# Optimization experiments

Hardware: AMD Instinct MI355X
Metric: run time of the kernel (lower is better)

Reference implementation:

```python
import jax, jax.numpy as jnp
import numpy as np
import math

B, T, S, C, E = 8, 2048, 2048, 1024, 1024

def setup_inputs() -> dict:
    key = jax.random.key(0)
    ks = jax.random.split(key, 6)
    x = jax.random.normal(ks[0], (B, T, C), dtype=jnp.float32)
    tgt = jax.random.normal(ks[1], (B, T, E), dtype=jnp.float32)
    enc_a = jax.random.normal(ks[2], (B, E, S), dtype=jnp.float32)
    enc_b = jax.random.normal(ks[3], (B, S, E), dtype=jnp.float32)
    mask = jax.random.randint(ks[4], (B, S), 0, 2).astype(bool)
    w_in = jax.random.normal(ks[5], (E, C), dtype=jnp.float32) * math.sqrt(1.0 / C)
    b_in = jnp.zeros((E,), dtype=jnp.float32)
    w_out = jax.random.normal(jax.random.fold_in(key, 7), (C, E), dtype=jnp.float32) * math.sqrt(1.0 / E)
    b_out = jnp.zeros((C,), dtype=jnp.float32)
    return {"x": x, "target_embedding": tgt, "encoder_a": enc_a, "encoder_b": enc_b,
            "encoder_padding_mask": mask, "w_in": w_in, "b_in": b_in,
            "w_out": w_out, "b_out": b_out}

def reference(x, target_embedding, encoder_a, encoder_b, encoder_padding_mask,
              w_in, b_in, w_out, b_out):
    residual = x
    h = (jnp.einsum('btc,ec->bte', x, w_in) + b_in + target_embedding) * math.sqrt(0.5)
    # attention scores: [B, T, S]
    scores = jnp.einsum('bte,bes->bts', h, encoder_a)
    scores = jnp.where(encoder_padding_mask[:, None, :], -jnp.inf, scores)
    attn = jax.nn.softmax(scores, axis=-1)
    out = jnp.einsum('bts,bse->bte', attn, encoder_b)
    s = encoder_b.shape[1]
    out = out * (s * math.sqrt(1.0 / s))
    out = (jnp.einsum('bte,ce->btc', out, w_out) + b_out + residual) * math.sqrt(0.5)
    return (out, attn)
```

## Files before the change

kernel.cpp:

```cpp
#include <hip/hip_runtime.h>
#include <hip/hip_bf16.h>
#include <math.h>

#define NB 8
#define TT 2048
#define SS 2048
#define CC 1024
#define EE 1024
#define NMAX 1280

typedef __attribute__((ext_vector_type(8))) short short8;
typedef __attribute__((ext_vector_type(4))) float f32x4;

__device__ __forceinline__ unsigned short f2bf(float f) {
  unsigned u = __builtin_bit_cast(unsigned, f);
  u += 0x7fffu + ((u >> 16) & 1u);
  return (unsigned short)(u >> 16);
}
__device__ __forceinline__ float bf2f(unsigned short h) {
  unsigned u = ((unsigned)h) << 16;
  return __builtin_bit_cast(float, u);
}
__device__ __forceinline__ void gload16(const void* g, void* l) {
  __builtin_amdgcn_global_load_lds((const __attribute__((address_space(1))) void*)g,
                                   (__attribute__((address_space(3))) void*)l, 16, 0, 0);
}
__device__ __forceinline__ unsigned ldsoff(const void* p) {
  return (unsigned)(size_t)(const __attribute__((address_space(3))) char*)p;
}
__device__ __forceinline__ short8 ds128(unsigned off) {
  short8 r;
  asm volatile("ds_read_b128 %0, %1" : "=v"(r) : "v"(off));
  return r;
}
__device__ __forceinline__ int swzi(int x) { return x ^ (((x >> 7) & 7) << 4); }

#define WAITV(N) asm volatile("s_waitcnt vmcnt(" #N ")" ::: "memory")
#define WAITL(N) asm volatile("s_waitcnt lgkmcnt(" #N ")" ::: "memory")
#define BAR() __builtin_amdgcn_s_barrier()
#define SCH0() __builtin_amdgcn_sched_barrier(0)
#define PRIO1() __builtin_amdgcn_s_setprio(1)
#define PRIO0() __builtin_amdgcn_s_setprio(0)
#define MF(a_, b_, c_) __builtin_amdgcn_mfma_f32_16x16x32_bf16(a_, b_, c_, 0, 0, 0)

__device__ __forceinline__ int xcd_logical() {
  int gx = gridDim.x, gy = gridDim.y, gz = gridDim.z;
  int pid = blockIdx.x + gx * (blockIdx.y + gy * blockIdx.z);
  int q = (gx * gy * gz) >> 3;
  return (pid & 7) * q + (pid >> 3);
}

__global__ __launch_bounds__(256) void k_scan(const int* __restrict__ mask,
    int* __restrict__ idx, int* __restrict__ pfx, int* __restrict__ cnt,
    int* __restrict__ kpad) {
  __shared__ int cs[256];
  int b = blockIdx.x, t = threadIdx.x;
  const int* mrow = mask + (size_t)b * SS;
  int4 a = ((const int4*)mrow)[t * 2];
  int4 c2 = ((const int4*)mrow)[t * 2 + 1];
  int mm[8] = {a.x, a.y, a.z, a.w, c2.x, c2.y, c2.z, c2.w};
  int c = 0;
#pragma unroll
  for (int j = 0; j < 8; ++j) c += (mm[j] == 0);
  cs[t] = c;
  __syncthreads();
  if (t == 0) {
    int run = 0;
    for (int i = 0; i < 256; ++i) { int tmp = cs[i]; cs[i] = run; run += tmp; }
    cnt[b] = run;
    int kp = (run + 127) & ~127;
    if (kp > NMAX) kp = NMAX;
    kpad[b] = kp;
  }
  __syncthreads();
  int base = cs[t];
#pragma unroll
  for (int j = 0; j < 8; ++j) {
    int s = t * 8 + j;
    pfx[(size_t)b * SS + s] = base;
    if (mm[j] == 0) { idx[(size_t)b * SS + base] = s; base++; }
  }
}

__global__ __launch_bounds__(256) void k_split(const float* __restrict__ in,
    unsigned short* __restrict__ hi, unsigned short* __restrict__ lo, long n4) {
  long i = (long)blockIdx.x * blockDim.x + threadIdx.x;
  long stride = (long)gridDim.x * blockDim.x;
  for (; i < n4; i += stride) {
    float4 v = ((const float4*)in)[i];
    float f[4] = {v.x, v.y, v.z, v.w};
    unsigned short hh[4], ll[4];
#pragma unroll
    for (int j = 0; j < 4; ++j) {
      hh[j] = f2bf(f[j]);
      ll[j] = f2bf(f[j] - bf2f(hh[j]));
    }
    ushort4 h; h.x = hh[0]; h.y = hh[1]; h.z = hh[2]; h.w = hh[3];
    ushort4 l; l.x = ll[0]; l.y = ll[1]; l.z = ll[2]; l.w = ll[3];
    ((ushort4*)hi)[i] = h;
    ((ushort4*)lo)[i] = l;
  }
}

__global__ __launch_bounds__(256) void k_conv(const float* __restrict__ in,
    unsigned short* __restrict__ out, long n4) {
  long i = (long)blockIdx.x * blockDim.x + threadIdx.x;
  long stride = (long)gridDim.x * blockDim.x;
  for (; i < n4; i += stride) {
    float4 v = ((const float4*)in)[i];
    ushort4 h; h.x = f2bf(v.x); h.y = f2bf(v.y); h.z = f2bf(v.z); h.w = f2bf(v.w);
    ((ushort4*)out)[i] = h;
  }
}

__global__ __launch_bounds__(256) void k_ta(const float* __restrict__ enca,
    const int* __restrict__ idx, const int* __restrict__ cnt,
    unsigned short* __restrict__ hi, unsigned short* __restrict__ lo) {
  __shared__ float tile[64][65];
  int b = blockIdx.z, sc0 = blockIdx.x * 64, e0 = blockIdx.y * 64;
  int cb = cnt[b];
  const float* src = enca + (size_t)b * EE * SS;
  int t = threadIdx.x, tr = t >> 4, tc = (t & 15) * 4;
  int idxv[4];
#pragma unroll
  for (int j = 0; j < 4; ++j) {
    int sc = sc0 + tc + j;
    idxv[j] = (sc < cb) ? idx[(size_t)b * SS + sc] : -1;
  }
#pragma unroll
  for (int i = 0; i < 4; ++i) {
    int e = tr + i * 16;
#pragma unroll
    for (int j = 0; j < 4; ++j)
      tile[e][tc + j] = (idxv[j] >= 0) ? src[(size_t)(e0 + e) * SS + idxv[j]] : 0.f;
  }
  __syncthreads();
  size_t ob = (size_t)b * NMAX * EE;
#pragma unroll
  for (int i = 0; i < 4; ++i) {
    int c = tr + i * 16;
    unsigned short hh[4], ll[4];
#pragma unroll
    for (int j = 0; j < 4; ++j) {
      float f = tile[tc + j][c];
      hh[j] = f2bf(f);
      ll[j] = f2bf(f - bf2f(hh[j]));
    }
    ushort4 h; h.x = hh[0]; h.y = hh[1]; h.z = hh[2]; h.w = hh[3];
    ushort4 l; l.x = ll[0]; l.y = ll[1]; l.z = ll[2]; l.w = ll[3];
    *(ushort4*)(hi + ob + (size_t)(sc0 + c) * EE + e0 + tc) = h;
    *(ushort4*)(lo + ob + (size_t)(sc0 + c) * EE + e0 + tc) = l;
  }
}

__global__ __launch_bounds__(256) void k_tb(const float* __restrict__ encb,
    const int* __restrict__ idx, const int* __restrict__ cnt,
    unsigned short* __restrict__ out) {
  __shared__ float tile[64][65];
  int b = blockIdx.z, sc0 = blockIdx.x * 64, e0 = blockIdx.y * 64;
  int cb = cnt[b];
  const float* src = encb + (size_t)b * SS * EE;
  int t = threadIdx.x, tr = t >> 4, tc = (t & 15) * 4;
#pragma unroll
  for (int i = 0; i < 4; ++i) {
    int r = tr + i * 16;
    int sc = sc0 + r;
    int sidx = (sc < cb) ? idx[(size_t)b * SS + sc] : -1;
    float4 v;
    if (sidx >= 0) v = *(const float4*)(src + (size_t)sidx * EE + e0 + tc);
    else { v.x = v.y = v.z = v.w = 0.f; }
    tile[r][tc] = v.x; tile[r][tc + 1] = v.y; tile[r][tc + 2] = v.z; tile[r][tc + 3] = v.w;
  }
  __syncthreads();
  size_t ob = (size_t)b * EE * NMAX;
#pragma unroll
  for (int i = 0; i < 4; ++i) {
    int c = tr + i * 16;
    unsigned short hh[4];
#pragma unroll
    for (int j = 0; j < 4; ++j) hh[j] = f2bf(tile[tc + j][c]);
    ushort4 h; h.x = hh[0]; h.y = hh[1]; h.z = hh[2]; h.w = hh[3];
    *(ushort4*)(out + ob + (size_t)(e0 + c) * NMAX + sc0 + tc) = h;
  }
}

template <int EPI>
__global__ __launch_bounds__(512, 2) void k_gemm8(
    const unsigned short* __restrict__ A, const unsigned short* __restrict__ B,
    int N, int KROW, const int* __restrict__ kdyn, long sA, long sB, long sC,
    const float* __restrict__ bias, const float* __restrict__ addend,
    float* __restrict__ outF, unsigned short* __restrict__ outH, float scale) {
  extern __shared__ char lds[];
  const int tid = threadIdx.x, wave = tid >> 6, lane = tid & 63;
  int L = xcd_logical();
  const int n0 = (L % gridDim.x) * 256;
  int tmpL = L / gridDim.x;
  const int m0 = (tmpL % gridDim.y) * 256;
  const int b = tmpL / gridDim.y;
  const int KD = kdyn ? kdyn[b] : KROW;
  const int wm = wave >> 2, wn = wave & 3;
  const unsigned short* gA = A + (size_t)b * sA + (size_t)m0 * KROW;
  const unsigned short* gB = B + (size_t)b * sB + (size_t)n0 * KROW;
  const unsigned ldsB = ldsoff(lds);

  int srow[2], sk8[2];
#pragma unroll
  for (int s = 0; s < 2; ++s) {
    int l = swzi((s * 512 + tid) * 16);
    srow[s] = l >> 6;
    sk8[s] = (l >> 4) & 3;
  }
  const int aR = wm * 128 + (lane & 15);
  const int bR = wn * 64 + (lane & 15);
  const int kB = (lane >> 4) * 16;
  const int nkt = KD >> 6;

  f32x4 acc[8][4] = {};

  auto STG = [&](int t, int tensor, int ks) {
    const unsigned short* g = tensor ? gB : gA;
    char* dst = lds + (t & 1) * 65536 + tensor * 32768 + ks * 16384 + wave * 1024;
    size_t gk = (size_t)t * 64 + ks * 32;
#pragma unroll
    for (int s = 0; s < 2; ++s)
      gload16(g + ((size_t)srow[s] * KROW + gk + sk8[s] * 8), dst + s * 8192);
  };
  auto RA = [&](int t, int ks, int mf) {
    int lin = (aR + mf * 16) * 64 + kB;
    return ds128(ldsB + (t & 1) * 65536 + ks * 16384 + swzi(lin));
  };
  auto RB = [&](int t, int ks, int nf) {
    int lin = (bR + nf * 16) * 64 + kB;
    return ds128(ldsB + (t & 1) * 65536 + 32768 + ks * 16384 + swzi(lin));
  };

  STG(0, 1, 0); STG(0, 0, 0); STG(0, 0, 1); STG(0, 1, 1);
  if (nkt > 1) { STG(1, 1, 0); STG(1, 0, 0); }

  for (int u = 0; u < nkt; ++u) {
    if (u + 1 < nkt) { WAITV(8); } else { WAITV(0); }
    BAR();
    short8 bf[4], af[4];
#pragma unroll
    for (int nf = 0; nf < 4; ++nf) bf[nf] = RB(u, 0, nf);
#pragma unroll
    for (int mf = 0; mf < 4; ++mf) af[mf] = RA(u, 0, mf);
    if (u + 1 < nkt) { STG(u + 1, 0, 1); STG(u + 1, 1, 1); }
    BAR(); WAITL(0); SCH0(); PRIO1();
#pragma unroll
    for (int mf = 0; mf < 4; ++mf)
#pragma unroll
      for (int nf = 0; nf < 4; ++nf) acc[mf][nf] = MF(af[mf], bf[nf], acc[mf][nf]);
    PRIO0(); SCH0(); BAR();
#pragma unroll
    for (int mf = 0; mf < 4; ++mf) af[mf] = RA(u, 0, mf + 4);
    if (u + 2 < nkt) STG(u + 2, 1, 0);
    BAR(); WAITL(0); SCH0(); PRIO1();
#pragma unroll
    for (int mf = 0; mf < 4; ++mf)
#pragma unroll
      for (int nf = 0; nf < 4; ++nf) acc[mf + 4][nf] = MF(af[mf], bf[nf], acc[mf + 4][nf]);
    PRIO0(); SCH0();
    if (u + 2 < nkt) { WAITV(10); } else if (u + 1 < nkt) { WAITV(8); } else { WAITV(0); }
    BAR();
#pragma unroll
    for (int nf = 0; nf < 4; ++nf) bf[nf] = RB(u, 1, nf);
#pragma unroll
    for (int mf = 0; mf < 4; ++mf) af[mf] = RA(u, 1, mf);
    if (u + 2 < nkt) STG(u + 2, 0, 0);
    BAR(); WAITL(0); SCH0(); PRIO1();
#pragma unroll
    for (int mf = 0; mf < 4; ++mf)
#pragma unroll
      for (int nf = 0; nf < 4; ++nf) acc[mf][nf] = MF(af[mf], bf[nf], acc[mf][nf]);
    PRIO0(); SCH0(); BAR();
#pragma unroll
    for (int mf = 0; mf < 4; ++mf) af[mf] = RA(u, 1, mf + 4);
    BAR(); WAITL(0); SCH0(); PRIO1();
#pragma unroll
    for (int mf = 0; mf < 4; ++mf)
#pragma unroll
      for (int nf = 0; nf < 4; ++nf) acc[mf + 4][nf] = MF(af[mf], bf[nf], acc[mf + 4][nf]);
    PRIO0(); SCH0(); BAR();
  }

  const size_t cb = (size_t)b * sC;
  const int mB = m0 + wm * 128 + ((lane >> 4) << 2);
  const int nB = n0 + wn * 64 + (lane & 15);
#pragma unroll
  for (int mf = 0; mf < 8; ++mf)
#pragma unroll
    for (int j = 0; j < 4; ++j) {
      int m = mB + mf * 16 + j;
#pragma unroll
      for (int nf = 0; nf < 4; ++nf) {
        int n = nB + nf * 16;
        float v = acc[mf][nf][j];
        size_t o = (size_t)m * N + n;
        if (EPI == 2) outH[cb + o] = f2bf(v * scale);
        else outF[o] = (v + bias[n] + addend[o]) * scale;
      }
    }
}

template <int EPI>
__global__ __launch_bounds__(512, 2) void k_split8(
    const unsigned short* __restrict__ Ah, const unsigned short* __restrict__ Al,
    const unsigned short* __restrict__ Bh, const unsigned short* __restrict__ Bl,
    int N, int K, long sA, long sB, long sC,
    const float* __restrict__ bias, const float* __restrict__ addend,
    float* __restrict__ outF, unsigned short* __restrict__ outHi,
    unsigned short* __restrict__ outLo, float scale, const int* __restrict__ npad) {
  extern __shared__ char lds[];
  const int tid = threadIdx.x, wave = tid >> 6, lane = tid & 63;
  int L = xcd_logical();
  const int n0 = (L % gridDim.x) * 256;
  int tmpL = L / gridDim.x;
  const int m0 = (tmpL % gridDim.y) * 256;
  const int b = tmpL / gridDim.y;
  if (npad && n0 >= npad[b]) return;
  const int wm = wave >> 2, wn = wave & 3;
  const unsigned short* gb[4];
  gb[0] = Ah + (size_t)b * sA + (size_t)m0 * K;
  gb[1] = Al + (size_t)b * sA + (size_t)m0 * K;
  gb[2] = Bh + (size_t)b * sB + (size_t)n0 * K;
  gb[3] = Bl + (size_t)b * sB + (size_t)n0 * K;
  const unsigned ldsB = ldsoff(lds);

  int soff[2];
#pragma unroll
  for (int s = 0; s < 2; ++s) {
    int l = swzi((s * 512 + tid) * 16);
    soff[s] = (l >> 6) * K + ((l >> 4) & 3) * 8;
  }
  const int aR = wm * 128 + (lane & 15);
  const int bR = wn * 64 + (lane & 15);
  const int kB = (lane >> 4) * 16;
  const int nkt = K >> 5;

  unsigned vA = ldsB + (unsigned)swzi(aR * 64 + kB);
  unsigned vB = ldsB + (unsigned)swzi(bR * 64 + kB);

  f32x4 acc[8][4] = {};

  auto STG2 = [&](int t, unsigned bufbase, int region) {
    char* dst = lds + bufbase + region * 16384 + tid * 16;
    const unsigned short* g = gb[region] + (size_t)t * 32;
#pragma unroll
    for (int s = 0; s < 2; ++s)
      gload16(g + soff[s], dst + s * 8192);
  };

#define PH_TOP() BAR()
#define PH_MID() BAR(); WAITL(0); SCH0(); PRIO1()
#define PH_END() PRIO0(); SCH0()

#define TILE(u, WV1, WV3, WV5, STAGE) do {                                     \
  short8 ahi[8], bhi[4], blo[4], alo[4];                                       \
                                                         \
  WV1; PH_TOP();                                                               \
  _Pragma("unroll") for (int q = 0; q < 4; ++q) bhi[q] = ds128(vB + 32768 + q * 1024); \
  _Pragma("unroll") for (int q = 0; q < 4; ++q) ahi[q] = ds128(vA + q * 1024); \
  if (STAGE) STG2((u) + 1, nbuf, 0);                                           \
  PH_MID();                                                                    \
  _Pragma("unroll") for (int mi = 0; mi < 4; ++mi)                             \
  _Pragma("unroll") for (int ni = 0; ni < 4; ++ni)                             \
    acc[mi][ni] = MF(ahi[mi], bhi[ni], acc[mi][ni]);                           \
  PH_END();                                                                    \
                                                         \
  PH_TOP();                                                                    \
  _Pragma("unroll") for (int q = 0; q < 4; ++q) ahi[4 + q] = ds128(vA + (4 + q) * 1024); \
  if (STAGE) STG2((u) + 1, nbuf, 2);                                           \
  PH_MID();                                                                    \
  _Pragma("unroll") for (int mi = 0; mi < 4; ++mi)                             \
  _Pragma("unroll") for (int ni = 0; ni < 4; ++ni)                             \
    acc[4 + mi][ni] = MF(ahi[4 + mi], bhi[ni], acc[4 + mi][ni]);               \
  PH_END();                                                                    \
                                                         \
  WV3; PH_TOP();                                                               \
  _Pragma("unroll") for (int q = 0; q < 4; ++q) blo[q] = ds128(vB + 49152 + q * 1024); \
  if (STAGE) STG2((u) + 1, nbuf, 3);                                           \
  PH_MID();                                                                    \
  _Pragma("unroll") for (int mi = 0; mi < 4; ++mi)                             \
  _Pragma("unroll") for (int ni = 0; ni < 4; ++ni)                             \
    acc[mi][ni] = MF(ahi[mi], blo[ni], acc[mi][ni]);                           \
  PH_END();                                                                    \
                                                         \
  PH_TOP();                                                                    \
  if (STAGE) STG2((u) + 1, nbuf, 1);                                           \
  PH_MID();                                                                    \
  _Pragma("unroll") for (int mi = 0; mi < 4; ++mi)                             \
  _Pragma("unroll") for (int ni = 0; ni < 4; ++ni)                             \
    acc[4 + mi][ni] = MF(ahi[4 + mi], blo[ni], acc[4 + mi][ni]);               \
  PH_END();                                                                    \
                                                         \
  WV5; PH_TOP();                                                               \
  _Pragma("unroll") for (int q = 0; q < 4; ++q) alo[q] = ds128(vA + 16384 + q * 1024); \
  PH_MID();                                                                    \
  _Pragma("unroll") for (int mi = 0; mi < 4; ++mi)                             \
  _Pragma("unroll") for (int ni = 0; ni < 4; ++ni)                             \
    acc[mi][ni] = MF(alo[mi], bhi[ni], acc[mi][ni]);                           \
  PH_END();                                                                    \
                                                         \
  PH_TOP();                                                                    \
  _Pragma("unroll") for (int q = 0; q < 4; ++q) alo[q] = ds128(vA + 16384 + (4 + q) * 1024); \
  PH_MID();                                                                    \
  _Pragma("unroll") for (int mi = 0; mi < 4; ++mi)                             \
  _Pragma("unroll") for (int ni = 0; ni < 4; ++ni)                             \
    acc[4 + mi][ni] = MF(alo[mi], bhi[ni], acc[4 + mi][ni]);                   \
  PH_END();                                                                    \
  vA ^= 65536u; vB ^= 65536u;                                                  \
} while (0)

  STG2(0, 0, 0); STG2(0, 0, 2); STG2(0, 0, 3); STG2(0, 0, 1);

  unsigned nbuf = 65536u;
  for (int u = 0; u < nkt - 1; ++u) {
    TILE(u, WAITV(4), WAITV(6), WAITV(8), 1);
    nbuf ^= 65536u;
  }
  TILE(nkt - 1, WAITV(4), WAITV(2), WAITV(0), 0);
#undef TILE
#undef PH_TOP
#undef PH_MID
#undef PH_END

  const size_t cb = (size_t)b * sC;
  const int mB = m0 + wm * 128 + ((lane >> 4) << 2);
  const int nB = n0 + wn * 64 + (lane & 15);
#pragma unroll
  for (int mf = 0; mf < 8; ++mf)
#pragma unroll
    for (int j = 0; j < 4; ++j) {
      int m = mB + mf * 16 + j;
#pragma unroll
      for (int nf = 0; nf < 4; ++nf) {
        int n = nB + nf * 16;
        float v = acc[mf][nf][j];
        size_t o = (size_t)m * N + n;
        if (EPI == 0) {
          v = (v + bias[n] + addend[o]) * scale;
          unsigned short hb = f2bf(v);
          outHi[o] = hb;
          outLo[o] = f2bf(v - bf2f(hb));
        } else {
          outF[cb + o] = v;
        }
      }
    }
}

__global__ __launch_bounds__(256) void k_softmax(const float* __restrict__ scores_c,
    float* __restrict__ attn, unsigned short* __restrict__ attn_bc,
    const int* __restrict__ mask, const int* __restrict__ pfx,
    const int* __restrict__ cnt, const int* __restrict__ kpad) {
  __shared__ float sl[NMAX];
  __shared__ float red[8];
  long r = blockIdx.x;
  int b = (int)(r >> 11);
  int t = threadIdx.x;
  int cb = cnt[b], kp = kpad[b];
  const float* srow = scores_c + r * (long)NMAX;
  for (int i = t; i < cb; i += 256) sl[i] = srow[i];
  __syncthreads();
  int base = t * 8;
  const int* mrow = mask + (size_t)b * SS;
  int4 m0i = *(const int4*)(mrow + base);
  int4 m1i = *(const int4*)(mrow + base + 4);
  int mm[8] = {m0i.x, m0i.y, m0i.z, m0i.w, m1i.x, m1i.y, m1i.z, m1i.w};
  const int* prow = pfx + (size_t)b * SS;
  int4 p0i = *(const int4*)(prow + base);
  int4 p1i = *(const int4*)(prow + base + 4);
  int pp[8] = {p0i.x, p0i.y, p0i.z, p0i.w, p1i.x, p1i.y, p1i.z, p1i.w};
  float v[8];
#pragma unroll
  for (int j = 0; j < 8; ++j) v[j] = mm[j] ? -INFINITY : sl[pp[j]];
  float mx = v[0];
#pragma unroll
  for (int j = 1; j < 8; ++j) mx = fmaxf(mx, v[j]);
#pragma unroll
  for (int off = 32; off; off >>= 1) mx = fmaxf(mx, __shfl_xor(mx, off));
  int wv = t >> 6, ln = t & 63;
  if (ln == 0) red[wv] = mx;
  __syncthreads();
  mx = fmaxf(fmaxf(red[0], red[1]), fmaxf(red[2], red[3]));
  float sum = 0.f;
#pragma unroll
  for (int j = 0; j < 8; ++j) { v[j] = __expf(v[j] - mx); sum += v[j]; }
#pragma unroll
  for (int off = 32; off; off >>= 1) sum += __shfl_xor(sum, off);
  if (ln == 0) red[4 + wv] = sum;
  __syncthreads();
  sum = (red[4] + red[5]) + (red[6] + red[7]);
  float inv = 1.0f / sum;
#pragma unroll
  for (int j = 0; j < 8; ++j) v[j] *= inv;
  float* arow = attn + r * (long)SS;
  float4 w0; w0.x = v[0]; w0.y = v[1]; w0.z = v[2]; w0.w = v[3];
  float4 w1; w1.x = v[4]; w1.y = v[5]; w1.z = v[6]; w1.w = v[7];
  *(float4*)(arow + base) = w0;
  *(float4*)(arow + base + 4) = w1;
  __syncthreads();
#pragma unroll
  for (int j = 0; j < 8; ++j) if (!mm[j]) sl[pp[j]] = v[j];
  __syncthreads();
  unsigned short* brow = attn_bc + r * (long)NMAX;
  for (int i = t; i < kp; i += 256) brow[i] = f2bf(i < cb ? sl[i] : 0.f);
}

extern "C" void kernel_launch(void* const* d_in, const int* in_sizes, int n_in,
                              void* d_out, int out_size, void* d_ws, size_t ws_size,
                              hipStream_t stream) {
  (void)in_sizes; (void)n_in; (void)out_size; (void)ws_size;
  const float* x     = (const float*)d_in[0];
  const float* tgt   = (const float*)d_in[1];
  const float* enca  = (const float*)d_in[2];
  const float* encb  = (const float*)d_in[3];
  const int*   mask  = (const int*)d_in[4];
  const float* w_in  = (const float*)d_in[5];
  const float* b_in  = (const float*)d_in[6];
  const float* w_out = (const float*)d_in[7];
  const float* b_out = (const float*)d_in[8];

  float* out  = (float*)d_out;
  float* attn = out + (size_t)NB * TT * CC;

  char* ws = (char*)d_ws;
  float*          scores_c = (float*)(ws + 0);
  unsigned short* x_hi   = (unsigned short*)(ws + 0);
  unsigned short* x_lo   = (unsigned short*)(ws + 33554432L);
  unsigned short* pv     = (unsigned short*)(ws + 0);
  unsigned short* h_hi   = (unsigned short*)(ws + 83886080L);
  unsigned short* h_lo   = (unsigned short*)(ws + 117440512L);
  unsigned short* attn_bc= (unsigned short*)(ws + 83886080L);
  unsigned short* a_tc_hi= (unsigned short*)(ws + 150994944L);
  unsigned short* a_tc_lo= (unsigned short*)(ws + 171966464L);
  unsigned short* b_tc   = (unsigned short*)(ws + 192937984L);
  unsigned short* w_in_hi= (unsigned short*)(ws + 213909504L);
  unsigned short* w_in_lo= (unsigned short*)(ws + 216006656L);
  unsigned short* w_out_b= (unsigned short*)(ws + 218103808L);
  int* idx  = (int*)(ws + 220200960L);
  int* pfx  = (int*)(ws + 220266496L);
  int* cnt  = (int*)(ws + 220332032L);
  int* kpad = (int*)(ws + 220332096L);

  hipFuncSetAttribute(reinterpret_cast<const void*>(&k_gemm8<2>),
                      hipFuncAttributeMaxDynamicSharedMemorySize, 131072);
  hipFuncSetAttribute(reinterpret_cast<const void*>(&k_gemm8<3>),
                      hipFuncAttributeMaxDynamicSharedMemorySize, 131072);
  hipFuncSetAttribute(reinterpret_cast<const void*>(&k_split8<0>),
                      hipFuncAttributeMaxDynamicSharedMemorySize, 131072);
  hipFuncSetAttribute(reinterpret_cast<const void*>(&k_split8<1>),
                      hipFuncAttributeMaxDynamicSharedMemorySize, 131072);

  dim3 blk(256), blk512(512);
  const float S05 = 0.70710678118654752f;

  k_scan<<<NB, blk, 0, stream>>>(mask, idx, pfx, cnt, kpad);
  k_split<<<2048, blk, 0, stream>>>(x, x_hi, x_lo, (long)NB * TT * CC / 4);
  k_split<<<512, blk, 0, stream>>>(w_in, w_in_hi, w_in_lo, (long)EE * CC / 4);
  k_conv<<<512, blk, 0, stream>>>(w_out, w_out_b, (long)CC * EE / 4);
  k_ta<<<dim3(NMAX / 64, EE / 64, NB), blk, 0, stream>>>(enca, idx, cnt, a_tc_hi, a_tc_lo);
  k_tb<<<dim3(NMAX / 64, EE / 64, NB), blk, 0, stream>>>(encb, idx, cnt, b_tc);

  k_split8<0><<<dim3(EE / 256, (NB * TT) / 256, 1), blk512, 131072, stream>>>(
      x_hi, x_lo, w_in_hi, w_in_lo, EE, CC, 0, 0, 0,
      b_in, tgt, nullptr, h_hi, h_lo, S05, nullptr);

  k_split8<1><<<dim3(NMAX / 256, TT / 256, NB), blk512, 131072, stream>>>(
      h_hi, h_lo, a_tc_hi, a_tc_lo, NMAX, EE,
      (long)TT * EE, (long)NMAX * EE, (long)TT * NMAX,
      nullptr, nullptr, scores_c, nullptr, nullptr, 1.0f, kpad);

  k_softmax<<<NB * TT, blk, 0, stream>>>(scores_c, attn, attn_bc, mask, pfx, cnt, kpad);

  k_gemm8<2><<<dim3(EE / 256, TT / 256, NB), blk512, 131072, stream>>>(
      attn_bc, b_tc, EE, NMAX, kpad,
      (long)TT * NMAX, (long)EE * NMAX, (long)TT * EE,
      nullptr, nullptr, nullptr, pv, 45.254833995939045f);

  k_gemm8<3><<<dim3(CC / 256, (NB * TT) / 256, 1), blk512, 131072, stream>>>(
      pv, w_out_b, CC, EE, nullptr, 0, 0, 0,
      b_out, x, out, nullptr, S05);
}
```

Baseline: 511.1 us.

## Shrink split-bf16 GEMM tile to 128x256 with single-buffered three-phase pipeline

Changes the split-precision (hi/lo bf16) GEMM kernel from 256x256 tiles with a double-buffered 128KB LDS pipeline to 128x256 tiles using a 48KB single-buffer scheme. Loads for the next k-step are interleaved into the three MFMA phases. Per-wave accumulators drop from 8x4 to 4x4. The goal is lower register and LDS pressure, higher occupancy and more blocks for better load balance. The cost is less A/B reuse per tile, more global traffic, and possible exposed latency with only one buffer.

```diff
diff --git a/kernel.cpp b/kernel.cpp
--- a/kernel.cpp
+++ b/kernel.cpp
@@ -316,7 +316,7 @@
   int L = xcd_logical();
   const int n0 = (L % gridDim.x) * 256;
   int tmpL = L / gridDim.x;
-  const int m0 = (tmpL % gridDim.y) * 256;
+  const int m0 = (tmpL % gridDim.y) * 128;
   const int b = tmpL / gridDim.y;
   if (npad && n0 >= npad[b]) return;
   const int wm = wave >> 2, wn = wave & 3;
@@ -327,109 +327,77 @@
   gb[3] = Bl + (size_t)b * sB + (size_t)n0 * K;
   const unsigned ldsB = ldsoff(lds);
 
-  int soff[2];
+  int aoff, boff[2];
+  { int l = swzi(tid * 16); aoff = (l >> 6) * K + ((l >> 4) & 3) * 8; }
 #pragma unroll
   for (int s = 0; s < 2; ++s) {
-    int l = swzi((s * 512 + tid) * 16);
-    soff[s] = (l >> 6) * K + ((l >> 4) & 3) * 8;
-  }
-  const int aR = wm * 128 + (lane & 15);
+    int l = swzi(s * 8192 + tid * 16);
+    boff[s] = (l >> 6) * K + ((l >> 4) & 3) * 8;
+  }
+  const int aR = wm * 64 + (lane & 15);
   const int bR = wn * 64 + (lane & 15);
   const int kB = (lane >> 4) * 16;
   const int nkt = K >> 5;
 
-  unsigned vA = ldsB + (unsigned)swzi(aR * 64 + kB);
-  unsigned vB = ldsB + (unsigned)swzi(bR * 64 + kB);
-
-  f32x4 acc[8][4] = {};
-
-  auto STG2 = [&](int t, unsigned bufbase, int region) {
-    char* dst = lds + bufbase + region * 16384 + tid * 16;
-    const unsigned short* g = gb[region] + (size_t)t * 32;
-#pragma unroll
-    for (int s = 0; s < 2; ++s)
-      gload16(g + soff[s], dst + s * 8192);
+  const unsigned vA = ldsB + (unsigned)swzi(aR * 64 + kB);
+  const unsigned vB = ldsB + 16384u + (unsigned)swzi(bR * 64 + kB);
+
+  f32x4 acc[4][4] = {};
+
+  auto STG_A = [&](int t, int r) {
+    gload16(gb[r] + (size_t)t * 32 + aoff, lds + r * 8192 + tid * 16);
   };
-
-#define PH_TOP() BAR()
-#define PH_MID() BAR(); WAITL(0); SCH0(); PRIO1()
-#define PH_END() PRIO0(); SCH0()
-
-#define TILE(u, WV1, WV3, WV5, STAGE) do {                                     \
-  short8 ahi[8], bhi[4], blo[4], alo[4];                                       \
-                                                         \
-  WV1; PH_TOP();                                                               \
-  _Pragma("unroll") for (int q = 0; q < 4; ++q) bhi[q] = ds128(vB + 32768 + q * 1024); \
+  auto STG_B = [&](int t, int r) {
+    char* base = lds + 16384 + (r - 2) * 16384;
+    const unsigned short* g = gb[r] + (size_t)t * 32;
+    gload16(g + boff[0], base + tid * 16);
+    gload16(g + boff[1], base + 8192 + tid * 16);
+  };
+
+#define TILE3(u, WV1, WV2, WV3, STAGE) do {                                    \
+  short8 ahi[4], bhi[4], blo[4], alo[4];                                       \
+                                                               \
+  WV1; BAR();                                                                  \
+  _Pragma("unroll") for (int q = 0; q < 4; ++q) bhi[q] = ds128(vB + q * 1024); \
   _Pragma("unroll") for (int q = 0; q < 4; ++q) ahi[q] = ds128(vA + q * 1024); \
-  if (STAGE) STG2((u) + 1, nbuf, 0);                                           \
-  PH_MID();                                                                    \
+  STG_A(u, 1);                                                                 \
+  BAR(); WAITL(0); SCH0(); PRIO1();                                            \
   _Pragma("unroll") for (int mi = 0; mi < 4; ++mi)                             \
   _Pragma("unroll") for (int ni = 0; ni < 4; ++ni)                             \
     acc[mi][ni] = MF(ahi[mi], bhi[ni], acc[mi][ni]);                           \
-  PH_END();                                                                    \
-                                                         \
-  PH_TOP();                                                                    \
-  _Pragma("unroll") for (int q = 0; q < 4; ++q) ahi[4 + q] = ds128(vA + (4 + q) * 1024); \
-  if (STAGE) STG2((u) + 1, nbuf, 2);                                           \
-  PH_MID();                                                                    \
-  _Pragma("unroll") for (int mi = 0; mi < 4; ++mi)                             \
-  _Pragma("unroll") for (int ni = 0; ni < 4; ++ni)                             \
-    acc[4 + mi][ni] = MF(ahi[4 + mi], bhi[ni], acc[4 + mi][ni]);               \
-  PH_END();                                                                    \
-                                                         \
-  WV3; PH_TOP();                                                               \
-  _Pragma("unroll") for (int q = 0; q < 4; ++q) blo[q] = ds128(vB + 49152 + q * 1024); \
-  if (STAGE) STG2((u) + 1, nbuf, 3);                                           \
-  PH_MID();                                                                    \
+  PRIO0(); SCH0();                                                             \
+                                                               \
+  WV2; BAR();                                                                  \
+  _Pragma("unroll") for (int q = 0; q < 4; ++q) blo[q] = ds128(vB + 16384 + q * 1024); \
+  if (STAGE) { STG_B((u) + 1, 2); STG_A((u) + 1, 0); }                         \
+  BAR(); WAITL(0); SCH0(); PRIO1();                                            \
   _Pragma("unroll") for (int mi = 0; mi < 4; ++mi)                             \
   _Pragma("unroll") for (int ni = 0; ni < 4; ++ni)                             \
     acc[mi][ni] = MF(ahi[mi], blo[ni], acc[mi][ni]);                           \
-  PH_END();                                                                    \
-                                                         \
-  PH_TOP();                                                                    \
-  if (STAGE) STG2((u) + 1, nbuf, 1);                                           \
-  PH_MID();                                                                    \
-  _Pragma("unroll") for (int mi = 0; mi < 4; ++mi)                             \
-  _Pragma("unroll") for (int ni = 0; ni < 4; ++ni)                             \
-    acc[4 + mi][ni] = MF(ahi[4 + mi], blo[ni], acc[4 + mi][ni]);               \
-  PH_END();                                                                    \
-                                                         \
-  WV5; PH_TOP();                                                               \
-  _Pragma("unroll") for (int q = 0; q < 4; ++q) alo[q] = ds128(vA + 16384 + q * 1024); \
-  PH_MID();                                                                    \
+  PRIO0(); SCH0();                                                             \
+                                                               \
+  WV3; BAR();                                                                  \
+  _Pragma("unroll") for (int q = 0; q < 4; ++q) alo[q] = ds128(vA + 8192 + q * 1024); \
+  if (STAGE) STG_B((u) + 1, 3);                                                \
+  BAR(); WAITL(0); SCH0(); PRIO1();                                            \
   _Pragma("unroll") for (int mi = 0; mi < 4; ++mi)                             \
   _Pragma("unroll") for (int ni = 0; ni < 4; ++ni)                             \
     acc[mi][ni] = MF(alo[mi], bhi[ni], acc[mi][ni]);                           \
-  PH_END();                                                                    \
-                                                         \
-  PH_TOP();                                                                    \
-  _Pragma("unroll") for (int q = 0; q < 4; ++q) alo[q] = ds128(vA + 16384 + (4 + q) * 1024); \
-  PH_MID();                                                                    \
-  _Pragma("unroll") for (int mi = 0; mi < 4; ++mi)                             \
-  _Pragma("unroll") for (int ni = 0; ni < 4; ++ni)                             \
-    acc[4 + mi][ni] = MF(alo[mi], bhi[ni], acc[4 + mi][ni]);                   \
-  PH_END();                                                                    \
-  vA ^= 65536u; vB ^= 65536u;                                                  \
+  PRIO0(); SCH0();                                                             \
 } while (0)
 
-  STG2(0, 0, 0); STG2(0, 0, 2); STG2(0, 0, 3); STG2(0, 0, 1);
-
-  unsigned nbuf = 65536u;
-  for (int u = 0; u < nkt - 1; ++u) {
-    TILE(u, WAITV(4), WAITV(6), WAITV(8), 1);
-    nbuf ^= 65536u;
-  }
-  TILE(nkt - 1, WAITV(4), WAITV(2), WAITV(0), 0);
-#undef TILE
-#undef PH_TOP
-#undef PH_MID
-#undef PH_END
+  STG_B(0, 2); STG_A(0, 0); STG_B(0, 3);
+
+  for (int u = 0; u < nkt - 1; ++u)
+    TILE3(u, WAITV(2), WAITV(1), WAITV(3), 1);
+  TILE3(nkt - 1, WAITV(2), WAITV(1), WAITV(0), 0);
+#undef TILE3
 
   const size_t cb = (size_t)b * sC;
-  const int mB = m0 + wm * 128 + ((lane >> 4) << 2);
+  const int mB = m0 + wm * 64 + ((lane >> 4) << 2);
   const int nB = n0 + wn * 64 + (lane & 15);
 #pragma unroll
-  for (int mf = 0; mf < 8; ++mf)
+  for (int mf = 0; mf < 4; ++mf)
 #pragma unroll
     for (int j = 0; j < 4; ++j) {
       int m = mB + mf * 16 + j;
@@ -549,9 +517,9 @@
   hipFuncSetAttribute(reinterpret_cast<const void*>(&k_gemm8<3>),
                       hipFuncAttributeMaxDynamicSharedMemorySize, 131072);
   hipFuncSetAttribute(reinterpret_cast<const void*>(&k_split8<0>),
-                      hipFuncAttributeMaxDynamicSharedMemorySize, 131072);
+                      hipFuncAttributeMaxDynamicSharedMemorySize, 49152);
   hipFuncSetAttribute(reinterpret_cast<const void*>(&k_split8<1>),
-                      hipFuncAttributeMaxDynamicSharedMemorySize, 131072);
+                      hipFuncAttributeMaxDynamicSharedMemorySize, 49152);
 
   dim3 blk(256), blk512(512);
   const float S05 = 0.70710678118654752f;
@@ -563,11 +531,11 @@
   k_ta<<<dim3(NMAX / 64, EE / 64, NB), blk, 0, stream>>>(enca, idx, cnt, a_tc_hi, a_tc_lo);
   k_tb<<<dim3(NMAX / 64, EE / 64, NB), blk, 0, stream>>>(encb, idx, cnt, b_tc);
 
-  k_split8<0><<<dim3(EE / 256, (NB * TT) / 256, 1), blk512, 131072, stream>>>(
+  k_split8<0><<<dim3(EE / 256, (NB * TT) / 128, 1), blk512, 49152, stream>>>(
       x_hi, x_lo, w_in_hi, w_in_lo, EE, CC, 0, 0, 0,
       b_in, tgt, nullptr, h_hi, h_lo, S05, nullptr);
 
-  k_split8<1><<<dim3(NMAX / 256, TT / 256, NB), blk512, 131072, stream>>>(
+  k_split8<1><<<dim3(NMAX / 256, TT / 128, NB), blk512, 49152, stream>>>(
       h_hi, h_lo, a_tc_hi, a_tc_lo, NMAX, EE,
       (long)TT * EE, (long)NMAX * EE, (long)TT * NMAX,
       nullptr, nullptr, scores_c, nullptr, nullptr, 1.0f, kpad);
```

Result: no change. 509.1 us (-0.4%).

## Add 128x256 split-bf16 score GEMM kernel with smaller LDS footprint

Applied to the files above, without the earlier changes.

Renames the existing split-precision GEMM to k_split6 and adds k_split3, a variant with 128-row M tiles, 4x4 accumulators per wave and a single-stage 48KB LDS buffer. The scores GEMM (h times encoder_a) now uses it. The smaller tile doubles the grid, which is meant to fill the GPU better, and the lower LDS use may let more blocks fit per CU. The kernel computes hi*hi + hi*lo + lo*hi, a 3-product split, and each staging step overlaps with the MFMAs. The cost is less data reuse per tile and more barriers per k-step, with no multi-stage buffering.

```diff
diff --git a/kernel.cpp b/kernel.cpp
--- a/kernel.cpp
+++ b/kernel.cpp
@@ -304,7 +304,7 @@
 }
 
 template <int EPI>
-__global__ __launch_bounds__(512, 2) void k_split8(
+__global__ __launch_bounds__(512, 2) void k_split6(
     const unsigned short* __restrict__ Ah, const unsigned short* __restrict__ Al,
     const unsigned short* __restrict__ Bh, const unsigned short* __restrict__ Bl,
     int N, int K, long sA, long sB, long sC,
@@ -450,6 +450,121 @@
     }
 }
 
+template <int EPI>
+__global__ __launch_bounds__(512, 2) void k_split3(
+    const unsigned short* __restrict__ Ah, const unsigned short* __restrict__ Al,
+    const unsigned short* __restrict__ Bh, const unsigned short* __restrict__ Bl,
+    int N, int K, long sA, long sB, long sC,
+    const float* __restrict__ bias, const float* __restrict__ addend,
+    float* __restrict__ outF, unsigned short* __restrict__ outHi,
+    unsigned short* __restrict__ outLo, float scale, const int* __restrict__ npad) {
+  extern __shared__ char lds[];
+  const int tid = threadIdx.x, wave = tid >> 6, lane = tid & 63;
+  int L = xcd_logical();
+  const int n0 = (L % gridDim.x) * 256;
+  int tmpL = L / gridDim.x;
+  const int m0 = (tmpL % gridDim.y) * 128;
+  const int b = tmpL / gridDim.y;
+  if (npad && n0 >= npad[b]) return;
+  const int wm = wave >> 2, wn = wave & 3;
+  const unsigned short* gb[4];
+  gb[0] = Ah + (size_t)b * sA + (size_t)m0 * K;
+  gb[1] = Al + (size_t)b * sA + (size_t)m0 * K;
+  gb[2] = Bh + (size_t)b * sB + (size_t)n0 * K;
+  gb[3] = Bl + (size_t)b * sB + (size_t)n0 * K;
+  const unsigned ldsB = ldsoff(lds);
+
+  int aoff, boff[2];
+  { int l = swzi(tid * 16); aoff = (l >> 6) * K + ((l >> 4) & 3) * 8; }
+#pragma unroll
+  for (int s = 0; s < 2; ++s) {
+    int l = swzi(s * 8192 + tid * 16);
+    boff[s] = (l >> 6) * K + ((l >> 4) & 3) * 8;
+  }
+  const int aR = wm * 64 + (lane & 15);
+  const int bR = wn * 64 + (lane & 15);
+  const int kB = (lane >> 4) * 16;
+  const int nkt = K >> 5;
+
+  const unsigned vA = ldsB + (unsigned)swzi(aR * 64 + kB);
+  const unsigned vB = ldsB + 16384u + (unsigned)swzi(bR * 64 + kB);
+
+  f32x4 acc[4][4] = {};
+
+  auto STG_A = [&](int t, int r) {
+    gload16(gb[r] + (size_t)t * 32 + aoff, lds + r * 8192 + tid * 16);
+  };
+  auto STG_B = [&](int t, int r) {
+    char* base = lds + 16384 + (r - 2) * 16384;
+    const unsigned short* g = gb[r] + (size_t)t * 32;
+    gload16(g + boff[0], base + tid * 16);
+    gload16(g + boff[1], base + 8192 + tid * 16);
+  };
+
+#define TILE3(u, WV1, WV2, WV3, STAGE) do {                                    \
+  short8 ahi[4], bhi[4], blo[4], alo[4];                                       \
+                                                               \
+  WV1; BAR();                                                                  \
+  _Pragma("unroll") for (int q = 0; q < 4; ++q) bhi[q] = ds128(vB + q * 1024); \
+  _Pragma("unroll") for (int q = 0; q < 4; ++q) ahi[q] = ds128(vA + q * 1024); \
+  STG_A(u, 1);                                                                 \
+  BAR(); WAITL(0); SCH0(); PRIO1();                                            \
+  _Pragma("unroll") for (int mi = 0; mi < 4; ++mi)                             \
+  _Pragma("unroll") for (int ni = 0; ni < 4; ++ni)                             \
+    acc[mi][ni] = MF(ahi[mi], bhi[ni], acc[mi][ni]);                           \
+  PRIO0(); SCH0();                                                             \
+                                                               \
+  WV2; BAR();                                                                  \
+  _Pragma("unroll") for (int q = 0; q < 4; ++q) blo[q] = ds128(vB + 16384 + q * 1024); \
+  if (STAGE) { STG_B((u) + 1, 2); STG_A((u) + 1, 0); }                         \
+  BAR(); WAITL(0); SCH0(); PRIO1();                                            \
+  _Pragma("unroll") for (int mi = 0; mi < 4; ++mi)                             \
+  _Pragma("unroll") for (int ni = 0; ni < 4; ++ni)                             \
+    acc[mi][ni] = MF(ahi[mi], blo[ni], acc[mi][ni]);                           \
+  PRIO0(); SCH0();                                                             \
+                                                               \
+  WV3; BAR();                                                                  \
+  _Pragma("unroll") for (int q = 0; q < 4; ++q) alo[q] = ds128(vA + 8192 + q * 1024); \
+  if (STAGE) STG_B((u) + 1, 3);                                                \
+  BAR(); WAITL(0); SCH0(); PRIO1();                                            \
+  _Pragma("unroll") for (int mi = 0; mi < 4; ++mi)                             \
+  _Pragma("unroll") for (int ni = 0; ni < 4; ++ni)                             \
+    acc[mi][ni] = MF(alo[mi], bhi[ni], acc[mi][ni]);                           \
+  PRIO0(); SCH0();                                                             \
+} while (0)
+
+  STG_B(0, 2); STG_A(0, 0); STG_B(0, 3);
+
+  for (int u = 0; u < nkt - 1; ++u)
+    TILE3(u, WAITV(2), WAITV(1), WAITV(3), 1);
+  TILE3(nkt - 1, WAITV(2), WAITV(1), WAITV(0), 0);
+#undef TILE3
+
+  const size_t cb = (size_t)b * sC;
+  const int mB = m0 + wm * 64 + ((lane >> 4) << 2);
+  const int nB = n0 + wn * 64 + (lane & 15);
+#pragma unroll
+  for (int mf = 0; mf < 4; ++mf)
+#pragma unroll
+    for (int j = 0; j < 4; ++j) {
+      int m = mB + mf * 16 + j;
+#pragma unroll
+      for (int nf = 0; nf < 4; ++nf) {
+        int n = nB + nf * 16;
+        float v = acc[mf][nf][j];
+        size_t o = (size_t)m * N + n;
+        if (EPI == 0) {
+          v = (v + bias[n] + addend[o]) * scale;
+          unsigned short hb = f2bf(v);
+          outHi[o] = hb;
+          outLo[o] = f2bf(v - bf2f(hb));
+        } else {
+          outF[cb + o] = v;
+        }
+      }
+    }
+}
+
 __global__ __launch_bounds__(256) void k_softmax(const float* __restrict__ scores_c,
     float* __restrict__ attn, unsigned short* __restrict__ attn_bc,
     const int* __restrict__ mask, const int* __restrict__ pfx,
@@ -548,10 +663,10 @@
                       hipFuncAttributeMaxDynamicSharedMemorySize, 131072);
   hipFuncSetAttribute(reinterpret_cast<const void*>(&k_gemm8<3>),
                       hipFuncAttributeMaxDynamicSharedMemorySize, 131072);
-  hipFuncSetAttribute(reinterpret_cast<const void*>(&k_split8<0>),
+  hipFuncSetAttribute(reinterpret_cast<const void*>(&k_split6<0>),
                       hipFuncAttributeMaxDynamicSharedMemorySize, 131072);
-  hipFuncSetAttribute(reinterpret_cast<const void*>(&k_split8<1>),
-                      hipFuncAttributeMaxDynamicSharedMemorySize, 131072);
+  hipFuncSetAttribute(reinterpret_cast<const void*>(&k_split3<1>),
+                      hipFuncAttributeMaxDynamicSharedMemorySize, 49152);
 
   dim3 blk(256), blk512(512);
   const float S05 = 0.70710678118654752f;
@@ -563,11 +678,11 @@
   k_ta<<<dim3(NMAX / 64, EE / 64, NB), blk, 0, stream>>>(enca, idx, cnt, a_tc_hi, a_tc_lo);
   k_tb<<<dim3(NMAX / 64, EE / 64, NB), blk, 0, stream>>>(encb, idx, cnt, b_tc);
 
-  k_split8<0><<<dim3(EE / 256, (NB * TT) / 256, 1), blk512, 131072, stream>>>(
+  k_split6<0><<<dim3(EE / 256, (NB * TT) / 256, 1), blk512, 131072, stream>>>(
       x_hi, x_lo, w_in_hi, w_in_lo, EE, CC, 0, 0, 0,
       b_in, tgt, nullptr, h_hi, h_lo, S05, nullptr);
 
-  k_split8<1><<<dim3(NMAX / 256, TT / 256, NB), blk512, 131072, stream>>>(
+  k_split3<1><<<dim3(NMAX / 256, TT / 128, NB), blk512, 49152, stream>>>(
       h_hi, h_lo, a_tc_hi, a_tc_lo, NMAX, EE,
       (long)TT * EE, (long)NMAX * EE, (long)TT * NMAX,
       nullptr, nullptr, scores_c, nullptr, nullptr, 1.0f, kpad);
```

New measurement: 496.8 us. -2.8%, faster.
